# Kernel optimization log

Hardware: AMD Instinct MI355X
Metric: run time of the kernel (lower is better)

The kernel has to match this reference:

```python
import jax, jax.numpy as jnp
import numpy as np

T, HQ, HKV, D, R = 2048, 16, 4, 128, 8
NEG = -1e30


def apply_rope(x, cos, sin):
    # x: [T, H, D]; cos/sin: [T, D//2]; non-interleaved rotary over full head dim
    c = jnp.concatenate([cos, cos], axis=-1)[:, None, :]  # [T,1,D]
    s = jnp.concatenate([sin, sin], axis=-1)[:, None, :]
    half = x.shape[-1] // 2
    x1, x2 = x[..., :half], x[..., half:]
    rot = jnp.concatenate([-x2, x1], axis=-1)
    return x * c + rot * s


def setup_inputs() -> dict:
    key = jax.random.key(0)
    kq, kk, kv = jax.random.split(key, 3)
    q = jax.random.normal(kq, (T, HQ, D), dtype=jnp.float32)
    k = jax.random.normal(kk, (T, HKV, D), dtype=jnp.float32)
    v = jax.random.normal(kv, (T, HKV, D), dtype=jnp.float32)
    # standard rotary tables
    inv_freq = 1.0 / (10000.0 ** (np.arange(0, D, 2, dtype=np.float32) / D))
    ang = np.arange(T, dtype=np.float32)[:, None] * inv_freq[None, :]  # [T, D/2]
    cos = jnp.asarray(np.cos(ang), dtype=jnp.float32)
    sin = jnp.asarray(np.sin(ang), dtype=jnp.float32)
    # block-causal ranges: q block r attends to keys [0, (r+1)*B)
    B = T // R
    q_ranges = jnp.asarray([[r * B, (r + 1) * B] for r in range(R)], dtype=jnp.int32)
    k_ranges = jnp.asarray([[0, (r + 1) * B] for r in range(R)], dtype=jnp.int32)
    return {"q": q, "k": k, "v": v, "cos": cos, "sin": sin,
            "q_ranges": q_ranges, "k_ranges": k_ranges}


def reference(q, k, v, cos, sin, q_ranges, k_ranges):
    scale = 1.0 / jnp.sqrt(jnp.float32(D))
    qh = apply_rope(q, cos, sin)
    kh = apply_rope(k, cos, sin)
    rep = HQ // HKV
    kr = jnp.repeat(kh, rep, axis=1)  # [T,HQ,D]
    vr = jnp.repeat(v, rep, axis=1)
    idx = jnp.arange(T)
    qm = (idx[None, :] >= q_ranges[:, :1]) & (idx[None, :] < q_ranges[:, 1:])  # [R,T]
    km = (idx[None, :] >= k_ranges[:, :1]) & (idx[None, :] < k_ranges[:, 1:])  # [R,T]
    mask = jnp.any(qm[:, :, None] & km[:, None, :], axis=0)  # [T,T] union over ranges
    scores = jnp.einsum('qhd,khd->hqk', qh, kr) * scale  # [HQ,T,T]
    scores = jnp.where(mask[None], scores, NEG)
    p = jax.nn.softmax(scores, axis=-1)
    row_valid = jnp.any(mask, axis=-1)  # [T]
    p = jnp.where(row_valid[None, :, None], p, 0.0)  # uncovered q rows output zero
    out = jnp.einsum('hqk,khd->qhd', p, vr)
    return out
```

## Files before the change

### kernel.cpp

```cpp
#include <hip/hip_runtime.h>
#include <hip/hip_bf16.h>

#define T_   2048
#define HQ_  16
#define HKV_ 4
#define D_   128
#define QBLK 64
#define NQB  (T_/QBLK)
#define KVBLK 32

typedef float f32x4 __attribute__((ext_vector_type(4)));
typedef __bf16 bf16x8 __attribute__((ext_vector_type(8)));
typedef unsigned short u16;
typedef unsigned short u16x8 __attribute__((ext_vector_type(8)));
typedef unsigned long long u64;
typedef unsigned u32;

__device__ __forceinline__ u16 f2bf(float f) {
  unsigned u = __builtin_bit_cast(unsigned, f);
  u += 0x7FFFu + ((u >> 16) & 1u);
  return (u16)(u >> 16);
}

#define QK_BLOCKS 1280
__global__ __launch_bounds__(256) void prep_all(
    const float* __restrict__ q, const float* __restrict__ k,
    const float* __restrict__ v, const float* __restrict__ ct,
    const float* __restrict__ st,
    u16* __restrict__ qr, u16* __restrict__ kr, u16* __restrict__ vt)
{
  __shared__ __attribute__((aligned(16))) char Lv[32 * 144];
  const int tid = threadIdx.x;
  const int bid = blockIdx.x;
  if (bid < QK_BLOCKS) {
    const float scale = 0.08838834764831845f;
    const int NQT = T_ * HQ_ * 8;
    int gid = bid * 256 + tid;
    if (gid < NQT) {
      int j0 = (gid & 7) * 8;
      int h  = (gid >> 3) & 15;
      int t  = gid >> 7;
      const float* base = q + ((size_t)t * HQ_ + h) * D_;
      const float* cb = ct + t * 64 + j0;
      const float* sb = st + t * 64 + j0;
      u16 lo[8], hi[8];
#pragma unroll
      for (int e = 0; e < 8; ++e) {
        float x1 = base[j0 + e], x2 = base[j0 + 64 + e];
        float c = cb[e], s = sb[e];
        lo[e] = f2bf((x1 * c - x2 * s) * scale);
        hi[e] = f2bf((x2 * c + x1 * s) * scale);
      }
      u16* orow = qr + ((size_t)h * T_ + t) * D_;
      *reinterpret_cast<u16x8*>(orow + j0)      = *reinterpret_cast<u16x8*>(lo);
      *reinterpret_cast<u16x8*>(orow + 64 + j0) = *reinterpret_cast<u16x8*>(hi);
    } else {
      int th = gid - NQT;
      int j0 = (th & 7) * 8;
      int hh = (th >> 3) & 3;
      int t  = th >> 5;
      const float* base = k + ((size_t)t * HKV_ + hh) * D_;
      const float* cb = ct + t * 64 + j0;
      const float* sb = st + t * 64 + j0;
      u16 lo[8], hi[8];
#pragma unroll
      for (int e = 0; e < 8; ++e) {
        float x1 = base[j0 + e], x2 = base[j0 + 64 + e];
        float c = cb[e], s = sb[e];
        lo[e] = f2bf(x1 * c - x2 * s);
        hi[e] = f2bf(x2 * c + x1 * s);
      }
      u16* orow = kr + ((size_t)hh * T_ + t) * D_;
      *reinterpret_cast<u16x8*>(orow + j0)      = *reinterpret_cast<u16x8*>(lo);
      *reinterpret_cast<u16x8*>(orow + 64 + j0) = *reinterpret_cast<u16x8*>(hi);
    }
  } else {
    int vbid = bid - QK_BLOCKS;
    int hh = vbid & 3;
    int t0 = ((vbid >> 2) & 31) * 64;
    int d0 = (vbid >> 7) * 32;
    {
      int r  = tid >> 2;
      int dg = tid & 3;
      const float* vrow = v + ((size_t)(t0 + r) * HKV_ + hh) * D_ + d0 + dg * 8;
      float4 f0 = *reinterpret_cast<const float4*>(vrow);
      float4 f1 = *reinterpret_cast<const float4*>(vrow + 4);
      float fv[8] = {f0.x, f0.y, f0.z, f0.w, f1.x, f1.y, f1.z, f1.w};
#pragma unroll
      for (int e = 0; e < 8; ++e)
        *reinterpret_cast<u16*>(Lv + (dg * 8 + e) * 144 + r * 2) = f2bf(fv[e]);
    }
    __syncthreads();
    {
      int dl = tid >> 3;
      int c0 = (tid & 7) * 16;
      u16x8 val = *reinterpret_cast<const u16x8*>(Lv + dl * 144 + c0);
      u16* orow = vt + ((size_t)(hh * D_ + d0 + dl)) * T_ + t0 + (c0 >> 1);
      *reinterpret_cast<u16x8*>(orow) = val;
    }
  }
}

__global__ __launch_bounds__(256, 4) void attn_fwd(
    const u16* __restrict__ qr, const u16* __restrict__ kr,
    const u16* __restrict__ vt, float* __restrict__ out)
{
  __shared__ __attribute__((aligned(16))) char lds[40960];

  const int tid  = threadIdx.x;
  const int lane = tid & 63;
  const int wv   = tid >> 6;
  char* Plds = lds + 32768 + wv * 2048;

  const int bid = blockIdx.x;
  const int f   = (bid ^ (bid >> 8)) & 1;
  const int x   = (bid >> 4) & 15;
  const int h   = ((bid >> 1) & 7) | (((bid >> 8) & 1) << 3);
  const int qb  = f ? (31 - x) : x;
  const int hkv = h >> 2;
  const int q0  = qb * QBLK + wv * 16;
  const int nt  = ((qb >> 2) + 1) * 8;

  const int lm = lane & 15;
  const int lh = lane >> 4;

  bf16x8 qf[4];
  {
    const u16* qrow = qr + ((size_t)h * T_ + q0 + lm) * D_;
#pragma unroll
    for (int kb = 0; kb < 4; ++kb)
      qf[kb] = *reinterpret_cast<const bf16x8*>(qrow + kb * 32 + lh * 8);
  }

  const u16* kbase = kr + (size_t)hkv * T_ * D_;
  const u16* vbase = vt + (size_t)hkv * D_ * T_;

  const int ks_row  = tid >> 4;
  const int ks_colb = (tid & 15) * 16;
  const int vs_d    = tid >> 1;
  const int vs_half = tid & 1;

  bf16x8 ksta[2], vsta[2];
#pragma unroll
  for (int j = 0; j < 2; ++j) {
    ksta[j] = *reinterpret_cast<const bf16x8*>(
        kbase + (size_t)(ks_row + j * 16) * D_ + (ks_colb >> 1));
    vsta[j] = *reinterpret_cast<const bf16x8*>(
        vbase + (size_t)vs_d * T_ + vs_half * 16 + j * 8);
  }

  f32x4 accO[8];
#pragma unroll
  for (int c = 0; c < 8; ++c) accO[c] = (f32x4){0.f, 0.f, 0.f, 0.f};
  float mrun = -1e30f, lrun = 0.f;

  for (int t = 0; t < nt; ++t) {
    char* Klds  = lds + (t & 1) * 8192;
    char* VTlds = lds + 16384 + (t & 1) * 8192;
#pragma unroll
    for (int j = 0; j < 2; ++j) {
      int row = ks_row + j * 16;
      int off = row * 256 + ks_colb;
      *reinterpret_cast<bf16x8*>(Klds + (off ^ ((row & 7) << 4))) = ksta[j];
      int prow = vs_d >> 1;
      int colb = (vs_d & 1) * 64 + vs_half * 32 + j * 16;
      *reinterpret_cast<bf16x8*>(
          VTlds + prow * 128 + (colb ^ ((prow & 7) << 4))) = vsta[j];
    }
    if (t + 1 < nt) {
      const int kv1 = (t + 1) * KVBLK;
#pragma unroll
      for (int j = 0; j < 2; ++j) {
        ksta[j] = *reinterpret_cast<const bf16x8*>(
            kbase + (size_t)(kv1 + ks_row + j * 16) * D_ + (ks_colb >> 1));
        vsta[j] = *reinterpret_cast<const bf16x8*>(
            vbase + (size_t)vs_d * T_ + kv1 + vs_half * 16 + j * 8);
      }
    }
    __syncthreads();

    f32x4 s[2];
#pragma unroll
    for (int g = 0; g < 2; ++g) s[g] = (f32x4){0.f, 0.f, 0.f, 0.f};
    __builtin_amdgcn_s_setprio(1);
#pragma unroll
    for (int kb = 0; kb < 4; ++kb) {
#pragma unroll
      for (int g = 0; g < 2; ++g) {
        int row = lm + 16 * g;
        bf16x8 kf = *reinterpret_cast<const bf16x8*>(
            Klds + ((row * 256 + kb * 64 + lh * 16) ^ ((row & 7) << 4)));
        s[g] = __builtin_amdgcn_mfma_f32_16x16x32_bf16(kf, qf[kb], s[g], 0, 0, 0);
      }
    }
    __builtin_amdgcn_s_setprio(0);

    float tmax = fmaxf(fmaxf(fmaxf(s[0][0], s[0][1]), fmaxf(s[0][2], s[0][3])),
                       fmaxf(fmaxf(s[1][0], s[1][1]), fmaxf(s[1][2], s[1][3])));
    tmax = fmaxf(tmax, __shfl_xor(tmax, 16));
    tmax = fmaxf(tmax, __shfl_xor(tmax, 32));
    float mnew  = fmaxf(mrun, tmax);
    float alpha = __expf(mrun - mnew);
    float psum = 0.f;
#pragma unroll
    for (int g = 0; g < 2; ++g) {
      float p0 = __expf(s[g][0] - mnew), p1 = __expf(s[g][1] - mnew);
      float p2 = __expf(s[g][2] - mnew), p3 = __expf(s[g][3] - mnew);
      psum += (p0 + p1) + (p2 + p3);
      u32 r01, r23;
      asm("v_cvt_pk_bf16_f32 %0, %1, %2" : "=v"(r01) : "v"(p0), "v"(p1));
      asm("v_cvt_pk_bf16_f32 %0, %1, %2" : "=v"(r23) : "v"(p2), "v"(p3));
      u64 w = (u64)r01 | ((u64)r23 << 32);
      *reinterpret_cast<u64*>(
          Plds + lm * 128 + ((g * 32 + lh * 8) ^ ((lm & 7) << 4))) = w;
    }
    psum += __shfl_xor(psum, 16);
    psum += __shfl_xor(psum, 32);
    lrun = lrun * alpha + psum;
    mrun = mnew;
#pragma unroll
    for (int c = 0; c < 8; ++c) {
      accO[c][0] *= alpha; accO[c][1] *= alpha;
      accO[c][2] *= alpha; accO[c][3] *= alpha;
    }

    bf16x8 pf = *reinterpret_cast<const bf16x8*>(
        Plds + lm * 128 + ((lh * 16) ^ ((lm & 7) << 4)));
    __builtin_amdgcn_s_setprio(1);
#pragma unroll
    for (int c = 0; c < 8; ++c) {
      int row  = c * 16 + lm;
      int prow = row >> 1;
      int colb = (row & 1) * 64 + lh * 16;
      bf16x8 vf = *reinterpret_cast<const bf16x8*>(
          VTlds + prow * 128 + (colb ^ ((prow & 7) << 4)));
      accO[c] = __builtin_amdgcn_mfma_f32_16x16x32_bf16(vf, pf, accO[c], 0, 0, 0);
    }
    __builtin_amdgcn_s_setprio(0);
  }

  float inv = 1.f / lrun;
  float* orow = out + ((size_t)(q0 + lm) * HQ_ + h) * D_ + lh * 4;
#pragma unroll
  for (int c = 0; c < 8; ++c) {
    f32x4 o;
    o[0] = accO[c][0] * inv; o[1] = accO[c][1] * inv;
    o[2] = accO[c][2] * inv; o[3] = accO[c][3] * inv;
    *reinterpret_cast<f32x4*>(orow + c * 16) = o;
  }
}

extern "C" void kernel_launch(void* const* d_in, const int* in_sizes, int n_in,
                              void* d_out, int out_size, void* d_ws, size_t ws_size,
                              hipStream_t stream) {
  const float* q  = (const float*)d_in[0];
  const float* k  = (const float*)d_in[1];
  const float* v  = (const float*)d_in[2];
  const float* ct = (const float*)d_in[3];
  const float* st = (const float*)d_in[4];

  u16* qr = (u16*)d_ws;
  u16* kr = qr + (size_t)T_ * HQ_ * D_;
  u16* vt = kr + (size_t)T_ * HKV_ * D_;
  float* out = (float*)d_out;

  prep_all<<<QK_BLOCKS + 512, 256, 0, stream>>>(q, k, v, ct, st, qr, kr, vt);
  attn_fwd<<<NQB * HQ_, 256, 0, stream>>>(qr, kr, vt, out);
}
```

Before: 134.0 us.

## Split attention KV range into fixed chunks with partial outputs and reduce kernel

Replaces the per-q-block variable-length KV loop with a split-KV scheme. Every workgroup now processes exactly 256 keys, and 2304 uniform workgroups are launched, grouped per KV head for locality. Partial outputs are written in bf16 together with max/sum stats, and a new reduce kernel combines them for q blocks that need more than one chunk. The aim is to remove the load imbalance of the triangular causal work and raise occupancy by shrinking LDS to a single buffer. The cost is an extra kernel launch, partial-result traffic, bf16 rounding of partials, and the loss of K/V double buffering.

```diff
diff --git a/kernel.cpp b/kernel.cpp
--- a/kernel.cpp
+++ b/kernel.cpp
@@ -6,7 +6,6 @@
 #define HKV_ 4
 #define D_   128
 #define QBLK 64
-#define NQB  (T_/QBLK)
 #define KVBLK 32
 
 typedef float f32x4 __attribute__((ext_vector_type(4)));
@@ -20,6 +19,9 @@
   unsigned u = __builtin_bit_cast(unsigned, f);
   u += 0x7FFFu + ((u >> 16) & 1u);
   return (u16)(u >> 16);
+}
+__device__ __forceinline__ float bf2f(u16 v) {
+  return __builtin_bit_cast(float, (u32)v << 16);
 }
 
 #define QK_BLOCKS 1280
@@ -101,25 +103,34 @@
   }
 }
 
-__global__ __launch_bounds__(256, 4) void attn_fwd(
+__global__ __launch_bounds__(256, 5) void attn_fwd(
     const u16* __restrict__ qr, const u16* __restrict__ kr,
-    const u16* __restrict__ vt, float* __restrict__ out)
+    const u16* __restrict__ vt, u16* __restrict__ part,
+    float* __restrict__ stats, float* __restrict__ out)
 {
-  __shared__ __attribute__((aligned(16))) char lds[40960];
+  __shared__ __attribute__((aligned(16))) char lds[24576];
+  char* Klds  = lds;
+  char* VTlds = lds + 8192;
 
   const int tid  = threadIdx.x;
   const int lane = tid & 63;
   const int wv   = tid >> 6;
-  char* Plds = lds + 32768 + wv * 2048;
+  char* Plds = lds + 16384 + wv * 2048;
 
   const int bid = blockIdx.x;
-  const int f   = (bid ^ (bid >> 8)) & 1;
-  const int x   = (bid >> 4) & 15;
-  const int h   = ((bid >> 1) & 7) | (((bid >> 8) & 1) << 3);
-  const int qb  = f ? (31 - x) : x;
-  const int hkv = h >> 2;
+  const int swz = (bid & 7) * 288 + (bid >> 3);
+  const int hkv = swz / 576;
+  const int rem = swz - hkv * 576;
+  const int pair = rem >> 2, hl = rem & 3;
+  int g = 0;
+  while (2 * (g + 1) * (g + 2) <= pair) ++g;
+  const int r   = pair - 2 * g * (g + 1);
+  const int cb1 = g + 1;
+  const int qb  = 4 * g + r / cb1;
+  const int ck  = r % cb1;
+  const int h   = hkv * 4 + hl;
   const int q0  = qb * QBLK + wv * 16;
-  const int nt  = ((qb >> 2) + 1) * 8;
+  const int kvbase = ck * 256;
 
   const int lm = lane & 15;
   const int lh = lane >> 4;
@@ -132,8 +143,8 @@
       qf[kb] = *reinterpret_cast<const bf16x8*>(qrow + kb * 32 + lh * 8);
   }
 
-  const u16* kbase = kr + (size_t)hkv * T_ * D_;
-  const u16* vbase = vt + (size_t)hkv * D_ * T_;
+  const u16* kbase = kr + ((size_t)hkv * T_ + kvbase) * D_;
+  const u16* vbase = vt + (size_t)hkv * D_ * T_ + kvbase;
 
   const int ks_row  = tid >> 4;
   const int ks_colb = (tid & 15) * 16;
@@ -154,9 +165,8 @@
   for (int c = 0; c < 8; ++c) accO[c] = (f32x4){0.f, 0.f, 0.f, 0.f};
   float mrun = -1e30f, lrun = 0.f;
 
-  for (int t = 0; t < nt; ++t) {
-    char* Klds  = lds + (t & 1) * 8192;
-    char* VTlds = lds + 16384 + (t & 1) * 8192;
+  for (int t = 0; t < 8; ++t) {
+    if (t > 0) __syncthreads();
 #pragma unroll
     for (int j = 0; j < 2; ++j) {
       int row = ks_row + j * 16;
@@ -167,7 +177,7 @@
       *reinterpret_cast<bf16x8*>(
           VTlds + prow * 128 + (colb ^ ((prow & 7) << 4))) = vsta[j];
     }
-    if (t + 1 < nt) {
+    if (t + 1 < 8) {
       const int kv1 = (t + 1) * KVBLK;
 #pragma unroll
       for (int j = 0; j < 2; ++j) {
@@ -181,16 +191,16 @@
 
     f32x4 s[2];
 #pragma unroll
-    for (int g = 0; g < 2; ++g) s[g] = (f32x4){0.f, 0.f, 0.f, 0.f};
+    for (int g2 = 0; g2 < 2; ++g2) s[g2] = (f32x4){0.f, 0.f, 0.f, 0.f};
     __builtin_amdgcn_s_setprio(1);
 #pragma unroll
     for (int kb = 0; kb < 4; ++kb) {
 #pragma unroll
-      for (int g = 0; g < 2; ++g) {
-        int row = lm + 16 * g;
+      for (int g2 = 0; g2 < 2; ++g2) {
+        int row = lm + 16 * g2;
         bf16x8 kf = *reinterpret_cast<const bf16x8*>(
             Klds + ((row * 256 + kb * 64 + lh * 16) ^ ((row & 7) << 4)));
-        s[g] = __builtin_amdgcn_mfma_f32_16x16x32_bf16(kf, qf[kb], s[g], 0, 0, 0);
+        s[g2] = __builtin_amdgcn_mfma_f32_16x16x32_bf16(kf, qf[kb], s[g2], 0, 0, 0);
       }
     }
     __builtin_amdgcn_s_setprio(0);
@@ -203,16 +213,16 @@
     float alpha = __expf(mrun - mnew);
     float psum = 0.f;
 #pragma unroll
-    for (int g = 0; g < 2; ++g) {
-      float p0 = __expf(s[g][0] - mnew), p1 = __expf(s[g][1] - mnew);
-      float p2 = __expf(s[g][2] - mnew), p3 = __expf(s[g][3] - mnew);
+    for (int g2 = 0; g2 < 2; ++g2) {
+      float p0 = __expf(s[g2][0] - mnew), p1 = __expf(s[g2][1] - mnew);
+      float p2 = __expf(s[g2][2] - mnew), p3 = __expf(s[g2][3] - mnew);
       psum += (p0 + p1) + (p2 + p3);
       u32 r01, r23;
       asm("v_cvt_pk_bf16_f32 %0, %1, %2" : "=v"(r01) : "v"(p0), "v"(p1));
       asm("v_cvt_pk_bf16_f32 %0, %1, %2" : "=v"(r23) : "v"(p2), "v"(p3));
       u64 w = (u64)r01 | ((u64)r23 << 32);
       *reinterpret_cast<u64*>(
-          Plds + lm * 128 + ((g * 32 + lh * 8) ^ ((lm & 7) << 4))) = w;
+          Plds + lm * 128 + ((g2 * 32 + lh * 8) ^ ((lm & 7) << 4))) = w;
     }
     psum += __shfl_xor(psum, 16);
     psum += __shfl_xor(psum, 32);
@@ -239,14 +249,91 @@
     __builtin_amdgcn_s_setprio(0);
   }
 
-  float inv = 1.f / lrun;
-  float* orow = out + ((size_t)(q0 + lm) * HQ_ + h) * D_ + lh * 4;
-#pragma unroll
-  for (int c = 0; c < 8; ++c) {
+  const int rowq = wv * 16 + lm;
+  if (g == 0) {
+    float inv = 1.f / lrun;
+    float* orow = out + ((size_t)(q0 + lm) * HQ_ + h) * D_ + lh * 4;
+#pragma unroll
+    for (int c = 0; c < 8; ++c) {
+      f32x4 o;
+      o[0] = accO[c][0] * inv; o[1] = accO[c][1] * inv;
+      o[2] = accO[c][2] * inv; o[3] = accO[c][3] * inv;
+      *reinterpret_cast<f32x4*>(orow + c * 16) = o;
+    }
+  } else {
+    u16* pp = part + (size_t)swz * 8192 + rowq * 128 + lh * 4;
+#pragma unroll
+    for (int c = 0; c < 8; ++c) {
+      u32 r01, r23;
+      asm("v_cvt_pk_bf16_f32 %0, %1, %2" : "=v"(r01) : "v"(accO[c][0]), "v"(accO[c][1]));
+      asm("v_cvt_pk_bf16_f32 %0, %1, %2" : "=v"(r23) : "v"(accO[c][2]), "v"(accO[c][3]));
+      u64 w = (u64)r01 | ((u64)r23 << 32);
+      *reinterpret_cast<u64*>(pp + c * 16) = w;
+    }
+    if (lh == 0) {
+      float2 ml = make_float2(mrun, lrun);
+      *reinterpret_cast<float2*>(stats + (size_t)swz * 128 + rowq * 2) = ml;
+    }
+  }
+}
+
+__global__ __launch_bounds__(256) void reduce_k(
+    const u16* __restrict__ part, const float* __restrict__ stats,
+    float* __restrict__ out)
+{
+  const int bid = blockIdx.x;
+  const int qb  = 4 + (bid >> 4);
+  const int h   = bid & 15;
+  const int hkv = h >> 2, hl = h & 3;
+  const int g   = qb >> 2;
+  const int cb  = g + 1;
+  const int pairbase = 2 * g * (g + 1) + (qb & 3) * cb;
+
+  const int t   = threadIdx.x;
+  const int row = t >> 2;
+  const int d0  = (t & 3) * 32;
+
+  float m[8], l[8];
+  float M = -1e30f;
+#pragma unroll
+  for (int c = 0; c < 8; ++c)
+    if (c < cb) {
+      int slot = hkv * 576 + (pairbase + c) * 4 + hl;
+      float2 ml = *reinterpret_cast<const float2*>(stats + (size_t)slot * 128 + row * 2);
+      m[c] = ml.x; l[c] = ml.y;
+      M = fmaxf(M, m[c]);
+    }
+  float L = 0.f;
+  float w[8];
+#pragma unroll
+  for (int c = 0; c < 8; ++c)
+    if (c < cb) { w[c] = __expf(m[c] - M); L += w[c] * l[c]; }
+  float inv = 1.f / L;
+
+  float acc[32];
+#pragma unroll
+  for (int e = 0; e < 32; ++e) acc[e] = 0.f;
+#pragma unroll
+  for (int c = 0; c < 8; ++c)
+    if (c < cb) {
+      int slot = hkv * 576 + (pairbase + c) * 4 + hl;
+      const u16* pr = part + (size_t)slot * 8192 + row * 128 + d0;
+      float wc = w[c];
+#pragma unroll
+      for (int j = 0; j < 4; ++j) {
+        u16x8 v = *reinterpret_cast<const u16x8*>(pr + j * 8);
+#pragma unroll
+        for (int e = 0; e < 8; ++e) acc[j * 8 + e] += wc * bf2f(v[e]);
+      }
+    }
+
+  float* orow = out + ((size_t)(qb * 64 + row) * HQ_ + h) * D_ + d0;
+#pragma unroll
+  for (int j = 0; j < 8; ++j) {
     f32x4 o;
-    o[0] = accO[c][0] * inv; o[1] = accO[c][1] * inv;
-    o[2] = accO[c][2] * inv; o[3] = accO[c][3] * inv;
-    *reinterpret_cast<f32x4*>(orow + c * 16) = o;
+    o[0] = acc[j * 4 + 0] * inv; o[1] = acc[j * 4 + 1] * inv;
+    o[2] = acc[j * 4 + 2] * inv; o[3] = acc[j * 4 + 3] * inv;
+    *reinterpret_cast<f32x4*>(orow + j * 4) = o;
   }
 }
 
@@ -262,8 +349,11 @@
   u16* qr = (u16*)d_ws;
   u16* kr = qr + (size_t)T_ * HQ_ * D_;
   u16* vt = kr + (size_t)T_ * HKV_ * D_;
+  u16* part = vt + (size_t)T_ * HKV_ * D_;
+  float* stats = (float*)(part + (size_t)2304 * 8192);
   float* out = (float*)d_out;
 
   prep_all<<<QK_BLOCKS + 512, 256, 0, stream>>>(q, k, v, ct, st, qr, kr, vt);
-  attn_fwd<<<NQB * HQ_, 256, 0, stream>>>(qr, kr, vt, out);
-}
+  attn_fwd<<<2304, 256, 0, stream>>>(qr, kr, vt, part, stats, out);
+  reduce_k<<<448, 256, 0, stream>>>(part, stats, out);
+}
```

Result: slower. 172.6 us (+28.8%).
